# Performance work log

Measured on AMD Instinct MI355X. Metric: run time of the kernel, lower is better.

## Reference

```python
import jax, jax.numpy as jnp
import numpy as np

N_SUBJECTS = 16
N_LABELS = 8
DENS_TEMP = 0.1  # args.ProtoSim_dens_temp


def setup_inputs() -> dict:
    key = jax.random.key(0)
    k1, k2, k3 = jax.random.split(key, 3)
    B, V, D = 131072, 2, 128
    X_data = jax.random.normal(k1, (B, V, D), dtype=jnp.float32)
    subject = jax.random.randint(k2, (B,), 0, N_SUBJECTS, dtype=jnp.int64) if jax.config.read('jax_enable_x64') else jax.random.randint(k2, (B,), 0, N_SUBJECTS)
    labels = jax.random.randint(k3, (B,), 0, N_LABELS)
    return {"X_data": X_data, "subject": subject, "labels": labels}


def reference(X_data, subject, labels):
    B, V, D = X_data.shape
    G = N_SUBJECTS * N_LABELS
    # torch.cat(torch.unbind(X_data, dim=1), dim=0): view-major ordering -> [V*B, D]
    cf = jnp.transpose(X_data, (1, 0, 2)).reshape(V * B, D)
    # subject/labels duplicated once (module assumes 2 views)
    seg = jnp.tile(subject * N_LABELS + labels, V)  # group id per row, [V*B]
    counts = jax.ops.segment_sum(jnp.ones((V * B,), jnp.float32), seg, num_segments=G)
    centroid = jax.ops.segment_sum(cf, seg, num_segments=G) / counts[:, None]  # [G, D]
    # per-point euclidean distance to own group centroid (torch.cdist to 1-row centroid)
    dist = jnp.linalg.norm(cf - centroid[seg], axis=1)  # [V*B]
    # density: mean(sqrt(dist)) / log(n + 10) for groups with n > 1, else 0 then dmax
    dens = (jax.ops.segment_sum(jnp.sqrt(dist), seg, num_segments=G) / counts) / jnp.log(counts + 10.0)
    dens = jnp.where(counts > 1, dens, 0.0)
    dens = jnp.where(counts > 1, dens, dens.max())
    lo = jnp.percentile(dens, 10.0)
    hi = jnp.percentile(dens, 90.0)
    dens = jnp.clip(dens, lo, hi)
    dens = DENS_TEMP * dens / dens.mean()
    cen_of_cen = centroid.mean(axis=0)  # [D]
    sim = jnp.exp((centroid @ cen_of_cen) / dens)  # [G]
    sim = sim - sim.max()
    return -sim.mean()
```

## Files before the change

kernel.cpp:

```cpp
#include <hip/hip_runtime.h>
#include <cstdint>
#include <cstddef>

#define BPTS    131072
#define D_DIM   128
#define G_GR    128
#define NL      8
#define GD      (G_GR * D_DIM)
#define NBLK    512
#define TPB     1024
#define PPB     (BPTS / NBLK)
#define GPW     (G_GR / (TPB / 64))
#define DRB     16

__device__ __forceinline__ float dpp_add(float d, const int ctrl) {
    int s;
    switch (ctrl) {
    case 0x111: s = __builtin_amdgcn_update_dpp(0, __float_as_int(d), 0x111, 0xf, 0xf, true); break;
    case 0x112: s = __builtin_amdgcn_update_dpp(0, __float_as_int(d), 0x112, 0xf, 0xf, true); break;
    case 0x114: s = __builtin_amdgcn_update_dpp(0, __float_as_int(d), 0x114, 0xf, 0xf, true); break;
    case 0x118: s = __builtin_amdgcn_update_dpp(0, __float_as_int(d), 0x118, 0xf, 0xf, true); break;
    case 0x142: s = __builtin_amdgcn_update_dpp(0, __float_as_int(d), 0x142, 0xf, 0xf, true); break;
    default:    s = __builtin_amdgcn_update_dpp(0, __float_as_int(d), 0x143, 0xf, 0xf, true); break;
    }
    return d + __int_as_float(s);
}

__device__ __forceinline__ float sum64(float d) {
    d = dpp_add(d, 0x111);
    d = dpp_add(d, 0x112);
    d = dpp_add(d, 0x114);
    d = dpp_add(d, 0x118);
    d = dpp_add(d, 0x142);
    d = dpp_add(d, 0x143);
    return d;
}

__device__ __forceinline__ void build_lists(const int* __restrict__ sub,
                                            const int* __restrict__ lab,
                                            int pbase, int t,
                                            int* glist, int* goff,
                                            int* hist, int* cursor, int* scan) {
    if (t < G_GR) hist[t] = 0;
    __syncthreads();
    int myg = -1;
    if (t < PPB) {
        myg = sub[pbase + t] * NL + lab[pbase + t];
        atomicAdd(&hist[myg], 1);
    }
    __syncthreads();
    if (t < G_GR) scan[t] = hist[t];
    __syncthreads();
    for (int s = 1; s < G_GR; s <<= 1) {
        int v = 0;
        if (t < G_GR) { v = scan[t]; if (t >= s) v += scan[t - s]; }
        __syncthreads();
        if (t < G_GR) scan[t] = v;
        __syncthreads();
    }
    if (t < G_GR) { goff[t] = scan[t] - hist[t]; cursor[t] = scan[t] - hist[t]; }
    __syncthreads();
    if (t < PPB) {
        int pos = atomicAdd(&cursor[myg], 1);
        glist[pos] = t;
    }
    __syncthreads();
}

__global__ __launch_bounds__(TPB) void k_centroid(const float* __restrict__ Xf,
                                                  const int* __restrict__ sub,
                                                  const int* __restrict__ lab,
                                                  float* __restrict__ cpart,
                                                  int* __restrict__ hpart) {
    __shared__ int glist[PPB];
    __shared__ int goff[G_GR];
    __shared__ int hist[G_GR];
    __shared__ int cursor[G_GR];
    __shared__ int scan[G_GR];
    int t = threadIdx.x, blk = blockIdx.x;
    int lane = t & 63, w = t >> 6;
    int pbase = blk * PPB;

    build_lists(sub, lab, pbase, t, glist, goff, hist, cursor, scan);
    if (t < G_GR) hpart[blk * G_GR + t] = hist[t];

    for (int gi = 0; gi < GPW; ++gi) {
        int g = w * GPW + gi;
        int s = goff[g], n = hist[g];
        float ax = 0.f, ay = 0.f;
        int k = 0;
        for (; k + 2 <= n; k += 2) {
            int p0 = pbase + glist[s + k];
            int p1 = pbase + glist[s + k + 1];
            const float* r0 = Xf + (size_t)p0 * 256;
            const float* r1 = Xf + (size_t)p1 * 256;
            float2 a0 = *(const float2*)(r0 + 2 * lane);
            float2 b0 = *(const float2*)(r0 + 128 + 2 * lane);
            float2 a1 = *(const float2*)(r1 + 2 * lane);
            float2 b1 = *(const float2*)(r1 + 128 + 2 * lane);
            ax += (a0.x + b0.x) + (a1.x + b1.x);
            ay += (a0.y + b0.y) + (a1.y + b1.y);
        }
        if (k < n) {
            int p = pbase + glist[s + k];
            const float* r = Xf + (size_t)p * 256;
            float2 a = *(const float2*)(r + 2 * lane);
            float2 b = *(const float2*)(r + 128 + 2 * lane);
            ax += a.x + b.x;
            ay += a.y + b.y;
        }
        float2 o; o.x = ax; o.y = ay;
        *(float2*)(cpart + (size_t)blk * GD + (size_t)g * D_DIM + 2 * lane) = o;
    }
}

__global__ __launch_bounds__(512) void k_reduce(const float* __restrict__ cpart,
                                                const int* __restrict__ hpart,
                                                float* __restrict__ centroid,
                                                float* __restrict__ countsf) {
    __shared__ float red[8][64];
    __shared__ int   hred[64];
    __shared__ float cf2s;
    int g = blockIdx.x >> 1, h = blockIdx.x & 1;
    int t = threadIdx.x;
    int dl = t & 63, bs = t >> 6;
    int d = h * 64 + dl;

    float acc = 0.f;
    for (int b = bs; b < NBLK; b += 8)
        acc += cpart[(size_t)b * GD + g * D_DIM + d];
    red[bs][dl] = acc;

    if (t < 64) {
        int hacc = 0;
        for (int b = t; b < NBLK; b += 64) hacc += hpart[b * G_GR + g];
        hred[t] = hacc;
    }
    __syncthreads();
    if (t == 0) {
        int n = 0;
        for (int i = 0; i < 64; ++i) n += hred[i];
        cf2s = 2.f * (float)n;
        if (h == 0) countsf[g] = cf2s;
    }
    __syncthreads();
    if (t < 64) {
        float v = 0.f;
#pragma unroll
        for (int r = 0; r < 8; ++r) v += red[r][t];
        float cf2 = cf2s;
        centroid[g * D_DIM + h * 64 + t] = (cf2 > 0.f) ? v / cf2 : 0.f;
    }
}

__global__ __launch_bounds__(TPB) void k_distn(const float* __restrict__ Xf,
                                               const int* __restrict__ sub,
                                               const int* __restrict__ lab,
                                               const float* __restrict__ centroid,
                                               float* __restrict__ dpart) {
    __shared__ int glist[PPB];
    __shared__ int goff[G_GR];
    __shared__ int hist[G_GR];
    __shared__ int cursor[G_GR];
    __shared__ int scan[G_GR];
    int t = threadIdx.x, blk = blockIdx.x;
    int lane = t & 63, w = t >> 6;
    int pbase = blk * PPB;

    build_lists(sub, lab, pbase, t, glist, goff, hist, cursor, scan);

    for (int gi = 0; gi < GPW; ++gi) {
        int g = w * GPW + gi;
        int s = goff[g], n = hist[g];
        float2 c = *(const float2*)(centroid + (size_t)g * D_DIM + 2 * lane);
        float sacc = 0.f;
        for (int k = 0; k < n; ++k) {
            int p = pbase + glist[s + k];
            const float* r = Xf + (size_t)p * 256;
            float2 a = *(const float2*)(r + 2 * lane);
            float2 b = *(const float2*)(r + 128 + 2 * lane);
            float e0 = a.x - c.x, e1 = a.y - c.y;
            float f0 = b.x - c.x, f1 = b.y - c.y;
            float d0 = sum64(e0 * e0 + e1 * e1);
            float d1 = sum64(f0 * f0 + f1 * f1);
            sacc += sqrtf(sqrtf(d0)) + sqrtf(sqrtf(d1));
        }
        if (lane == 63) dpart[blk * G_GR + g] = sacc;
    }
}

__global__ __launch_bounds__(256) void k_dred(const float* __restrict__ dpart,
                                              float* __restrict__ dmid) {
    __shared__ float red[2][G_GR];
    int t = threadIdx.x, blk = blockIdx.x;
    int d = t & 127, h = t >> 7;
    int b0 = blk * (NBLK / DRB);
    float acc = 0.f;
    for (int b = b0 + h; b < b0 + NBLK / DRB; b += 2)
        acc += dpart[b * G_GR + d];
    red[h][d] = acc;
    __syncthreads();
    if (t < G_GR) dmid[blk * G_GR + t] = red[0][t] + red[1][t];
}

__global__ __launch_bounds__(128) void k_final(const float* __restrict__ dmid,
                                               const float* __restrict__ countsf,
                                               const float* __restrict__ centroid,
                                               float* __restrict__ out) {
    __shared__ float srt[G_GR];
    __shared__ float red[G_GR];
    __shared__ float coc[D_DIM];
    int t = threadIdx.x;

    float ds = 0.f;
    for (int b = 0; b < DRB; ++b) ds += dmid[b * G_GR + t];
    float cnt  = countsf[t];
    float dens = (cnt > 1.f) ? (ds / cnt) / logf(cnt + 10.f) : 0.f;

    red[t] = dens;
    __syncthreads();
    for (int s = 64; s > 0; s >>= 1) {
        if (t < s) red[t] = fmaxf(red[t], red[t + s]);
        __syncthreads();
    }
    float dmax = red[0];
    __syncthreads();
    if (!(cnt > 1.f)) dens = dmax;

    srt[t] = dens;
    __syncthreads();
    for (int k = 2; k <= G_GR; k <<= 1) {
        for (int j = k >> 1; j > 0; j >>= 1) {
            int ixj = t ^ j;
            if (ixj > t) {
                float a = srt[t], b = srt[ixj];
                bool up = ((t & k) == 0);
                if ((a > b) == up) { srt[t] = b; srt[ixj] = a; }
            }
            __syncthreads();
        }
    }
    double p10 = 0.10 * 127.0, p90 = 0.90 * 127.0;
    int   i10 = (int)p10,           i90 = (int)p90;
    float f10 = (float)(p10 - i10), f90 = (float)(p90 - i90);
    float lo = srt[i10] + f10 * (srt[i10 + 1] - srt[i10]);
    float hi = srt[i90] + f90 * (srt[i90 + 1] - srt[i90]);
    dens = fminf(fmaxf(dens, lo), hi);

    red[t] = dens;
    __syncthreads();
    for (int s = 64; s > 0; s >>= 1) {
        if (t < s) red[t] += red[t + s];
        __syncthreads();
    }
    float dmean = red[0] / 128.f;
    __syncthreads();
    dens = 0.1f * dens / dmean;

    float cs = 0.f;
    for (int g = 0; g < G_GR; ++g) cs += centroid[g * D_DIM + t];
    coc[t] = cs / 128.f;
    __syncthreads();

    float dot = 0.f;
    for (int d = 0; d < D_DIM; ++d) dot += centroid[t * D_DIM + d] * coc[d];
    float sim = expf(dot / dens);

    red[t] = sim;
    __syncthreads();
    for (int s = 64; s > 0; s >>= 1) {
        if (t < s) red[t] = fmaxf(red[t], red[t + s]);
        __syncthreads();
    }
    float smax = red[0];
    __syncthreads();
    red[t] = sim - smax;
    __syncthreads();
    for (int s = 64; s > 0; s >>= 1) {
        if (t < s) red[t] += red[t + s];
        __syncthreads();
    }
    if (t == 0) out[0] = -(red[0] / 128.f);
}

extern "C" void kernel_launch(void* const* d_in, const int* in_sizes, int n_in,
                              void* d_out, int out_size, void* d_ws, size_t ws_size,
                              hipStream_t stream) {
    const float*  Xf      = (const float*)d_in[0];
    const int*    subject = (const int*)d_in[1];
    const int*    labels  = (const int*)d_in[2];
    float*        out     = (float*)d_out;
    char*         ws      = (char*)d_ws;

    size_t o = 0;
    float* cpart    = (float*)(ws + o); o += (size_t)NBLK * GD * 4;
    int*   hpart    = (int*)(ws + o);   o += (size_t)NBLK * G_GR * 4;
    float* centroid = (float*)(ws + o); o += (size_t)GD * 4;
    float* countsf  = (float*)(ws + o); o += 512;
    float* dpart    = (float*)(ws + o); o += (size_t)NBLK * G_GR * 4;
    float* dmid     = (float*)(ws + o); o += (size_t)DRB * G_GR * 4;

    k_centroid<<<NBLK, TPB, 0, stream>>>(Xf, subject, labels, cpart, hpart);
    k_reduce  <<<G_GR * 2, 512, 0, stream>>>(cpart, hpart, centroid, countsf);
    k_distn   <<<NBLK, TPB, 0, stream>>>(Xf, subject, labels, centroid, dpart);
    k_dred    <<<DRB, 256, 0, stream>>>(dpart, dmid);
    k_final   <<<1, 128, 0, stream>>>(dmid, countsf, centroid, out);
}
```

Before: 271.4 us.

## Halve block count, reuse per-block group lists, and merge the distance reduction into the final kernel

```diff
diff --git a/kernel.cpp b/kernel.cpp
--- a/kernel.cpp
+++ b/kernel.cpp
@@ -7,11 +7,10 @@
 #define G_GR    128
 #define NL      8
 #define GD      (G_GR * D_DIM)
-#define NBLK    512
+#define NBLK    256
 #define TPB     1024
 #define PPB     (BPTS / NBLK)
 #define GPW     (G_GR / (TPB / 64))
-#define DRB     16
 
 __device__ __forceinline__ float dpp_add(float d, const int ctrl) {
     int s;
@@ -36,42 +35,13 @@
     return d;
 }
 
-__device__ __forceinline__ void build_lists(const int* __restrict__ sub,
-                                            const int* __restrict__ lab,
-                                            int pbase, int t,
-                                            int* glist, int* goff,
-                                            int* hist, int* cursor, int* scan) {
-    if (t < G_GR) hist[t] = 0;
-    __syncthreads();
-    int myg = -1;
-    if (t < PPB) {
-        myg = sub[pbase + t] * NL + lab[pbase + t];
-        atomicAdd(&hist[myg], 1);
-    }
-    __syncthreads();
-    if (t < G_GR) scan[t] = hist[t];
-    __syncthreads();
-    for (int s = 1; s < G_GR; s <<= 1) {
-        int v = 0;
-        if (t < G_GR) { v = scan[t]; if (t >= s) v += scan[t - s]; }
-        __syncthreads();
-        if (t < G_GR) scan[t] = v;
-        __syncthreads();
-    }
-    if (t < G_GR) { goff[t] = scan[t] - hist[t]; cursor[t] = scan[t] - hist[t]; }
-    __syncthreads();
-    if (t < PPB) {
-        int pos = atomicAdd(&cursor[myg], 1);
-        glist[pos] = t;
-    }
-    __syncthreads();
-}
-
 __global__ __launch_bounds__(TPB) void k_centroid(const float* __restrict__ Xf,
                                                   const int* __restrict__ sub,
                                                   const int* __restrict__ lab,
                                                   float* __restrict__ cpart,
-                                                  int* __restrict__ hpart) {
+                                                  int* __restrict__ hpart,
+                                                  int* __restrict__ goffG,
+                                                  int* __restrict__ glistG) {
     __shared__ int glist[PPB];
     __shared__ int goff[G_GR];
     __shared__ int hist[G_GR];
@@ -81,27 +51,63 @@
     int lane = t & 63, w = t >> 6;
     int pbase = blk * PPB;
 
-    build_lists(sub, lab, pbase, t, glist, goff, hist, cursor, scan);
-    if (t < G_GR) hpart[blk * G_GR + t] = hist[t];
+    if (t < G_GR) hist[t] = 0;
+    __syncthreads();
+    int myg = -1;
+    if (t < PPB) {
+        myg = sub[pbase + t] * NL + lab[pbase + t];
+        atomicAdd(&hist[myg], 1);
+    }
+    __syncthreads();
+    if (t < G_GR) scan[t] = hist[t];
+    __syncthreads();
+    for (int s = 1; s < G_GR; s <<= 1) {
+        int v = 0;
+        if (t < G_GR) { v = scan[t]; if (t >= s) v += scan[t - s]; }
+        __syncthreads();
+        if (t < G_GR) scan[t] = v;
+        __syncthreads();
+    }
+    if (t < G_GR) { goff[t] = scan[t] - hist[t]; cursor[t] = scan[t] - hist[t]; }
+    __syncthreads();
+    if (t < PPB) {
+        int pos = atomicAdd(&cursor[myg], 1);
+        glist[pos] = t;
+    }
+    __syncthreads();
+
+    if (t < G_GR) {
+        hpart[blk * G_GR + t] = hist[t];
+        goffG[blk * G_GR + t] = goff[t];
+    }
+    if (t < PPB) glistG[blk * PPB + t] = glist[t];
 
     for (int gi = 0; gi < GPW; ++gi) {
         int g = w * GPW + gi;
         int s = goff[g], n = hist[g];
         float ax = 0.f, ay = 0.f;
         int k = 0;
-        for (; k + 2 <= n; k += 2) {
-            int p0 = pbase + glist[s + k];
+        for (; k + 4 <= n; k += 4) {
+            int p0 = pbase + glist[s + k + 0];
             int p1 = pbase + glist[s + k + 1];
+            int p2 = pbase + glist[s + k + 2];
+            int p3 = pbase + glist[s + k + 3];
             const float* r0 = Xf + (size_t)p0 * 256;
             const float* r1 = Xf + (size_t)p1 * 256;
+            const float* r2 = Xf + (size_t)p2 * 256;
+            const float* r3 = Xf + (size_t)p3 * 256;
             float2 a0 = *(const float2*)(r0 + 2 * lane);
             float2 b0 = *(const float2*)(r0 + 128 + 2 * lane);
             float2 a1 = *(const float2*)(r1 + 2 * lane);
             float2 b1 = *(const float2*)(r1 + 128 + 2 * lane);
-            ax += (a0.x + b0.x) + (a1.x + b1.x);
-            ay += (a0.y + b0.y) + (a1.y + b1.y);
-        }
-        if (k < n) {
+            float2 a2 = *(const float2*)(r2 + 2 * lane);
+            float2 b2 = *(const float2*)(r2 + 128 + 2 * lane);
+            float2 a3 = *(const float2*)(r3 + 2 * lane);
+            float2 b3 = *(const float2*)(r3 + 128 + 2 * lane);
+            ax += (a0.x + b0.x) + (a1.x + b1.x) + (a2.x + b2.x) + (a3.x + b3.x);
+            ay += (a0.y + b0.y) + (a1.y + b1.y) + (a2.y + b2.y) + (a3.y + b3.y);
+        }
+        for (; k < n; ++k) {
             int p = pbase + glist[s + k];
             const float* r = Xf + (size_t)p * 256;
             float2 a = *(const float2*)(r + 2 * lane);
@@ -126,10 +132,14 @@
     int dl = t & 63, bs = t >> 6;
     int d = h * 64 + dl;
 
-    float acc = 0.f;
-    for (int b = bs; b < NBLK; b += 8)
-        acc += cpart[(size_t)b * GD + g * D_DIM + d];
-    red[bs][dl] = acc;
+    float a0 = 0.f, a1 = 0.f, a2 = 0.f, a3 = 0.f;
+    for (int b = bs; b < NBLK; b += 32) {
+        a0 += cpart[(size_t)(b)      * GD + g * D_DIM + d];
+        a1 += cpart[(size_t)(b + 8)  * GD + g * D_DIM + d];
+        a2 += cpart[(size_t)(b + 16) * GD + g * D_DIM + d];
+        a3 += cpart[(size_t)(b + 24) * GD + g * D_DIM + d];
+    }
+    red[bs][dl] = (a0 + a1) + (a2 + a3);
 
     if (t < 64) {
         int hacc = 0;
@@ -154,27 +164,52 @@
 }
 
 __global__ __launch_bounds__(TPB) void k_distn(const float* __restrict__ Xf,
-                                               const int* __restrict__ sub,
-                                               const int* __restrict__ lab,
+                                               const int* __restrict__ hpart,
+                                               const int* __restrict__ goffG,
+                                               const int* __restrict__ glistG,
                                                const float* __restrict__ centroid,
                                                float* __restrict__ dpart) {
     __shared__ int glist[PPB];
     __shared__ int goff[G_GR];
     __shared__ int hist[G_GR];
-    __shared__ int cursor[G_GR];
-    __shared__ int scan[G_GR];
     int t = threadIdx.x, blk = blockIdx.x;
     int lane = t & 63, w = t >> 6;
     int pbase = blk * PPB;
 
-    build_lists(sub, lab, pbase, t, glist, goff, hist, cursor, scan);
+    if (t < G_GR) {
+        hist[t] = hpart[blk * G_GR + t];
+        goff[t] = goffG[blk * G_GR + t];
+    }
+    if (t < PPB) glist[t] = glistG[blk * PPB + t];
+    __syncthreads();
 
     for (int gi = 0; gi < GPW; ++gi) {
         int g = w * GPW + gi;
         int s = goff[g], n = hist[g];
         float2 c = *(const float2*)(centroid + (size_t)g * D_DIM + 2 * lane);
         float sacc = 0.f;
-        for (int k = 0; k < n; ++k) {
+        int k = 0;
+        for (; k + 2 <= n; k += 2) {
+            int p0 = pbase + glist[s + k];
+            int p1 = pbase + glist[s + k + 1];
+            const float* r0 = Xf + (size_t)p0 * 256;
+            const float* r1 = Xf + (size_t)p1 * 256;
+            float2 a0 = *(const float2*)(r0 + 2 * lane);
+            float2 b0 = *(const float2*)(r0 + 128 + 2 * lane);
+            float2 a1 = *(const float2*)(r1 + 2 * lane);
+            float2 b1 = *(const float2*)(r1 + 128 + 2 * lane);
+            float e0 = a0.x - c.x, e1 = a0.y - c.y;
+            float f0 = b0.x - c.x, f1 = b0.y - c.y;
+            float g0 = a1.x - c.x, g1 = a1.y - c.y;
+            float h0 = b1.x - c.x, h1 = b1.y - c.y;
+            float d0 = sum64(e0 * e0 + e1 * e1);
+            float d1 = sum64(f0 * f0 + f1 * f1);
+            float d2 = sum64(g0 * g0 + g1 * g1);
+            float d3 = sum64(h0 * h0 + h1 * h1);
+            sacc += (sqrtf(sqrtf(d0)) + sqrtf(sqrtf(d1)))
+                  + (sqrtf(sqrtf(d2)) + sqrtf(sqrtf(d3)));
+        }
+        if (k < n) {
             int p = pbase + glist[s + k];
             const float* r = Xf + (size_t)p * 256;
             float2 a = *(const float2*)(r + 2 * lane);
@@ -189,35 +224,35 @@
     }
 }
 
-__global__ __launch_bounds__(256) void k_dred(const float* __restrict__ dpart,
-                                              float* __restrict__ dmid) {
-    __shared__ float red[2][G_GR];
-    int t = threadIdx.x, blk = blockIdx.x;
-    int d = t & 127, h = t >> 7;
-    int b0 = blk * (NBLK / DRB);
-    float acc = 0.f;
-    for (int b = b0 + h; b < b0 + NBLK / DRB; b += 2)
-        acc += dpart[b * G_GR + d];
-    red[h][d] = acc;
-    __syncthreads();
-    if (t < G_GR) dmid[blk * G_GR + t] = red[0][t] + red[1][t];
-}
-
-__global__ __launch_bounds__(128) void k_final(const float* __restrict__ dmid,
+__global__ __launch_bounds__(512) void k_final(const float* __restrict__ dpart,
                                                const float* __restrict__ countsf,
                                                const float* __restrict__ centroid,
                                                float* __restrict__ out) {
+    __shared__ float sl4[4][G_GR];
     __shared__ float srt[G_GR];
     __shared__ float red[G_GR];
-    __shared__ float coc[D_DIM];
+    __shared__ float cocs[D_DIM];
+    __shared__ float dotv[G_GR];
+    __shared__ float densv[G_GR];
     int t = threadIdx.x;
-
-    float ds = 0.f;
-    for (int b = 0; b < DRB; ++b) ds += dmid[b * G_GR + t];
-    float cnt  = countsf[t];
-    float dens = (cnt > 1.f) ? (ds / cnt) / logf(cnt + 10.f) : 0.f;
-
-    red[t] = dens;
+    int col = t & 127, q = t >> 7;
+    int lane = t & 63, w8 = t >> 6;
+
+    float a0 = 0.f, a1 = 0.f;
+    for (int b = q; b < NBLK; b += 8) {
+        a0 += dpart[(b)     * G_GR + col];
+        a1 += dpart[(b + 4) * G_GR + col];
+    }
+    sl4[q][col] = a0 + a1;
+    __syncthreads();
+
+    float dens = 0.f, cnt = 0.f;
+    if (t < G_GR) {
+        float ds = sl4[0][t] + sl4[1][t] + sl4[2][t] + sl4[3][t];
+        cnt = countsf[t];
+        dens = (cnt > 1.f) ? (ds / cnt) / logf(cnt + 10.f) : 0.f;
+        red[t] = dens;
+    }
     __syncthreads();
     for (int s = 64; s > 0; s >>= 1) {
         if (t < s) red[t] = fmaxf(red[t], red[t + s]);
@@ -225,14 +260,14 @@
     }
     float dmax = red[0];
     __syncthreads();
-    if (!(cnt > 1.f)) dens = dmax;
-
-    srt[t] = dens;
+    if (t < G_GR && !(cnt > 1.f)) dens = dmax;
+
+    if (t < G_GR) srt[t] = dens;
     __syncthreads();
     for (int k = 2; k <= G_GR; k <<= 1) {
         for (int j = k >> 1; j > 0; j >>= 1) {
             int ixj = t ^ j;
-            if (ixj > t) {
+            if (t < G_GR && ixj > t) {
                 float a = srt[t], b = srt[ixj];
                 bool up = ((t & k) == 0);
                 if ((a > b) == up) { srt[t] = b; srt[ixj] = a; }
@@ -245,9 +280,9 @@
     float f10 = (float)(p10 - i10), f90 = (float)(p90 - i90);
     float lo = srt[i10] + f10 * (srt[i10 + 1] - srt[i10]);
     float hi = srt[i90] + f90 * (srt[i90 + 1] - srt[i90]);
-    dens = fminf(fmaxf(dens, lo), hi);
-
-    red[t] = dens;
+    if (t < G_GR) dens = fminf(fmaxf(dens, lo), hi);
+
+    if (t < G_GR) red[t] = dens;
     __syncthreads();
     for (int s = 64; s > 0; s >>= 1) {
         if (t < s) red[t] += red[t + s];
@@ -255,18 +290,33 @@
     }
     float dmean = red[0] / 128.f;
     __syncthreads();
-    dens = 0.1f * dens / dmean;
+    if (t < G_GR) densv[t] = 0.1f * dens / dmean;
 
     float cs = 0.f;
-    for (int g = 0; g < G_GR; ++g) cs += centroid[g * D_DIM + t];
-    coc[t] = cs / 128.f;
-    __syncthreads();
-
-    float dot = 0.f;
-    for (int d = 0; d < D_DIM; ++d) dot += centroid[t * D_DIM + d] * coc[d];
-    float sim = expf(dot / dens);
-
-    red[t] = sim;
+    for (int g = q; g < G_GR; g += 4) cs += centroid[g * D_DIM + col];
+    sl4[q][col] = cs;
+    __syncthreads();
+    if (t < D_DIM)
+        cocs[t] = (sl4[0][t] + sl4[1][t] + sl4[2][t] + sl4[3][t]) / 128.f;
+    __syncthreads();
+
+    {
+        float2 co = *(const float2*)&cocs[2 * lane];
+        for (int i = 0; i < 16; ++i) {
+            int g = w8 * 16 + i;
+            float2 c = *(const float2*)(centroid + (size_t)g * D_DIM + 2 * lane);
+            float p = c.x * co.x + c.y * co.y;
+            float s = sum64(p);
+            if (lane == 63) dotv[g] = s;
+        }
+    }
+    __syncthreads();
+
+    float sim = 0.f;
+    if (t < G_GR) {
+        sim = expf(dotv[t] / densv[t]);
+        red[t] = sim;
+    }
     __syncthreads();
     for (int s = 64; s > 0; s >>= 1) {
         if (t < s) red[t] = fmaxf(red[t], red[t + s]);
@@ -274,7 +324,7 @@
     }
     float smax = red[0];
     __syncthreads();
-    red[t] = sim - smax;
+    if (t < G_GR) red[t] = sim - smax;
     __syncthreads();
     for (int s = 64; s > 0; s >>= 1) {
         if (t < s) red[t] += red[t + s];
@@ -295,14 +345,14 @@
     size_t o = 0;
     float* cpart    = (float*)(ws + o); o += (size_t)NBLK * GD * 4;
     int*   hpart    = (int*)(ws + o);   o += (size_t)NBLK * G_GR * 4;
+    int*   goffG    = (int*)(ws + o);   o += (size_t)NBLK * G_GR * 4;
+    int*   glistG   = (int*)(ws + o);   o += (size_t)NBLK * PPB * 4;
     float* centroid = (float*)(ws + o); o += (size_t)GD * 4;
     float* countsf  = (float*)(ws + o); o += 512;
     float* dpart    = (float*)(ws + o); o += (size_t)NBLK * G_GR * 4;
-    float* dmid     = (float*)(ws + o); o += (size_t)DRB * G_GR * 4;
-
-    k_centroid<<<NBLK, TPB, 0, stream>>>(Xf, subject, labels, cpart, hpart);
+
+    k_centroid<<<NBLK, TPB, 0, stream>>>(Xf, subject, labels, cpart, hpart, goffG, glistG);
     k_reduce  <<<G_GR * 2, 512, 0, stream>>>(cpart, hpart, centroid, countsf);
-    k_distn   <<<NBLK, TPB, 0, stream>>>(Xf, subject, labels, centroid, dpart);
-    k_dred    <<<DRB, 256, 0, stream>>>(dpart, dmid);
-    k_final   <<<1, 128, 0, stream>>>(dmid, countsf, centroid, out);
-}
+    k_distn   <<<NBLK, TPB, 0, stream>>>(Xf, hpart, goffG, glistG, centroid, dpart);
+    k_final   <<<1, 512, 0, stream>>>(dpart, countsf, centroid, out);
+}
```

After: 264.8 us. -2.4%, faster.
